# Performance work log

Hardware: AMD Instinct MI355X
Metric: run time of the kernel (lower is better)

## Reference

```python
import jax, jax.numpy as jnp
import numpy as np

N = 1_000_000
G = 32
CLAMP = 1e-4          # sigmoid_clamp
GAMMA = 2.0           # module-level gamma
FOCAL_ALPHA = 0.25    # cfg.MODEL.FCOS.LOSS_ALPHA
FOCAL_GAMMA = 2.0     # cfg.MODEL.FCOS.LOSS_GAMMA


def setup_inputs() -> dict:
    key = jax.random.key(0)
    k1, k2, k3, k4 = jax.random.split(key, 4)
    return {
        "logits_pred": jax.random.normal(k1, (N, 1), dtype=jnp.float32),
        "scores": jax.random.uniform(k2, (N, 1), dtype=jnp.float32),
        "IoUMap": jax.random.uniform(k3, (N, 1), dtype=jnp.float32),
        "is_in_boxes": jax.random.randint(k4, (N, G), 0, 2, dtype=jnp.int32),
        "num_pos_avg": 100,
    }


def reference(logits_pred, scores, IoUMap, is_in_boxes, num_pos_avg):
    f32 = jnp.float32
    mask = is_in_boxes > 0                                  # [N,G] bool
    any_mask = mask.any(axis=0)                             # [G]

    p = jnp.clip(jax.nn.sigmoid(logits_pred), CLAMP, 1.0 - CLAMP)  # box_pred [N,1]
    p0 = p[:, 0]                                            # [N]

    # alignment metrics: single class => scores[:, labels] broadcasts column 0
    am = scores[:, 0][:, None] * mask.astype(f32)           # [N,G]
    iou = jax.lax.stop_gradient(IoUMap)[:, 0][:, None] * mask.astype(f32)

    # per-box confidence = max of alignment metric over in-box locations
    conf = jnp.max(jnp.where(mask, am, -jnp.inf), axis=0)   # [G]
    conf = jnp.where(any_mask, conf, f32(0.0))

    am_safe = jnp.where(mask, am, f32(1.0))                 # avoid pow(0, c) grad issues
    raw = jnp.where(mask, jnp.power(am_safe, conf[None, :]) * iou, f32(0.0))

    # normalize(x) = (x + 1e-4) / (max(x) + 1e-4) over in-box subset
    mx = jnp.max(jnp.where(mask, raw, -jnp.inf), axis=0)    # [G]
    mx = jnp.where(any_mask, mx, f32(1.0))
    pos_w = jnp.where(mask & any_mask[None, :],
                      (raw + CLAMP) / (mx[None, :] + CLAMP), f32(0.0))  # [N,G]

    # negative mask: locations covered by no gt box (single-class case)
    neg_mask = ~mask.any(axis=1)                            # [N]
    neg_loss = jnp.sum(jnp.where(neg_mask,
                                 -jnp.log(1.0 - p0) * jnp.power(p0, FOCAL_GAMMA),
                                 f32(0.0))) * (1.0 - FOCAL_ALPHA)

    wmask = pos_w > 0.0
    wc = jnp.clip(pos_w, CLAMP, 1.0 - CLAMP)                # clamp applied at positive entries
    logp = jnp.log(p0)[:, None]
    log1mp = jnp.log(1.0 - p0)[:, None]
    pos_loss = -jnp.sum(jnp.where(wmask,
                                  logp * jnp.power(wc * (1.0 - p0)[:, None], GAMMA),
                                  f32(0.0))) * FOCAL_ALPHA
    box_neg_loss = -jnp.sum(jnp.where(wmask,
                                      log1mp * jnp.power((1.0 - wc) * p0[:, None], GAMMA),
                                      f32(0.0))) * FOCAL_ALPHA

    denom = jnp.asarray(num_pos_avg, f32)
    return (neg_loss + pos_loss + box_neg_loss) / denom
```

## Files before the change

kernel.cpp:

```cpp
#include <hip/hip_runtime.h>
#include <hip/hip_bf16.h>
#include <stdint.h>


constexpr float kClamp = 1e-4f;

__global__ void init_kernel(uint32_t* confbits, uint32_t* mxbits, float* out) {
    int t = threadIdx.x;
    if (t < 32) { confbits[t] = 0u; mxbits[t] = 0u; }
    if (t == 0) out[0] = 0.0f;
}

template <bool WRITE_BITS>
__global__ void pack_conf_kernel(const int4* __restrict__ boxes4,
                                 const float* __restrict__ scores,
                                 uint32_t* __restrict__ bits,
                                 uint32_t* __restrict__ confbits,
                                 long long nchunks) {
    __shared__ uint32_t conf_lds[32];
    int tid = threadIdx.x;
    if (tid < 32) conf_lds[tid] = 0u;
    __syncthreads();
    long long stride = (long long)gridDim.x * blockDim.x;
    for (long long c = (long long)blockIdx.x * blockDim.x + tid; c < nchunks; c += stride) {
        int4 v = boxes4[c];
        uint32_t nib = (uint32_t)(v.x > 0) | ((uint32_t)(v.y > 0) << 1) |
                       ((uint32_t)(v.z > 0) << 2) | ((uint32_t)(v.w > 0) << 3);
        int sub = (int)(c & 7);
        long long row = c >> 3;
        if (WRITE_BITS) {
            uint32_t r = nib << (sub * 4);
            r |= __shfl_xor(r, 1);
            r |= __shfl_xor(r, 2);
            r |= __shfl_xor(r, 4);
            if ((tid & 7) == 0) bits[row] = r;
        }
        if (nib) {
            uint32_t sb = __float_as_uint(scores[row]);
            int g0 = sub * 4;
            if (nib & 1u) atomicMax(&conf_lds[g0 + 0], sb);
            if (nib & 2u) atomicMax(&conf_lds[g0 + 1], sb);
            if (nib & 4u) atomicMax(&conf_lds[g0 + 2], sb);
            if (nib & 8u) atomicMax(&conf_lds[g0 + 3], sb);
        }
    }
    __syncthreads();
    if (tid < 32 && conf_lds[tid]) atomicMax(&confbits[tid], conf_lds[tid]);
}

__device__ inline uint32_t row_mask_from_boxes(const int4* __restrict__ boxes4, int row) {
    uint32_t m = 0;
#pragma unroll
    for (int k = 0; k < 8; ++k) {
        int4 v = boxes4[(long long)row * 8 + k];
        uint32_t nib = (uint32_t)(v.x > 0) | ((uint32_t)(v.y > 0) << 1) |
                       ((uint32_t)(v.z > 0) << 2) | ((uint32_t)(v.w > 0) << 3);
        m |= nib << (k * 4);
    }
    return m;
}

template <bool USE_BITS>
__global__ void mx_kernel(const uint32_t* __restrict__ bits,
                          const int4* __restrict__ boxes4,
                          const float* __restrict__ scores,
                          const float* __restrict__ iouMap,
                          const uint32_t* __restrict__ confbits,
                          uint32_t* __restrict__ mxbits, int n) {
    __shared__ float conf_lds[32];
    __shared__ uint32_t mx_lds[32];
    int tid = threadIdx.x;
    if (tid < 32) { conf_lds[tid] = __uint_as_float(confbits[tid]); mx_lds[tid] = 0u; }
    __syncthreads();
    int stride = gridDim.x * blockDim.x;
    for (int row = blockIdx.x * blockDim.x + tid; row < n; row += stride) {
        uint32_t m = USE_BITS ? bits[row] : row_mask_from_boxes(boxes4, row);
        if (!m) continue;
        float s = scores[row];
        float iou = iouMap[row];
        float l2s = log2f(s);
        while (m) {
            int g = __ffs(m) - 1;
            m &= m - 1;
            float t = conf_lds[g] * l2s;
            float e = exp2f(t);
            if (t != t) e = 1.0f;
            float raw = e * iou;
            atomicMax(&mx_lds[g], __float_as_uint(raw));
        }
    }
    __syncthreads();
    if (tid < 32 && mx_lds[tid]) atomicMax(&mxbits[tid], mx_lds[tid]);
}

template <bool USE_BITS>
__global__ void loss_kernel(const uint32_t* __restrict__ bits,
                            const int4* __restrict__ boxes4,
                            const float* __restrict__ logits,
                            const float* __restrict__ scores,
                            const float* __restrict__ iouMap,
                            const uint32_t* __restrict__ confbits,
                            const uint32_t* __restrict__ mxbits,
                            const void* __restrict__ denom_ptr,
                            float* __restrict__ out, int n) {
    __shared__ float conf_lds[32];
    __shared__ float mx_lds[32];
    __shared__ float wsum[4];
    int tid = threadIdx.x;
    if (tid < 32) {
        conf_lds[tid] = __uint_as_float(confbits[tid]);
        mx_lds[tid] = __uint_as_float(mxbits[tid]);
    }
    __syncthreads();
    float acc = 0.0f;
    int stride = gridDim.x * blockDim.x;
    for (int row = blockIdx.x * blockDim.x + tid; row < n; row += stride) {
        uint32_t m = USE_BITS ? bits[row] : row_mask_from_boxes(boxes4, row);
        float x = logits[row];
        float p = 1.0f / (1.0f + expf(-x));
        p = fminf(fmaxf(p, kClamp), 1.0f - kClamp);
        if (!m) {
            float l1mp = logf(1.0f - p);
            acc -= l1mp * p * p * 0.75f;
            continue;
        }
        float s = scores[row];
        float iou = iouMap[row];
        float l2s = log2f(s);
        float logp = logf(p);
        float log1mp = logf(1.0f - p);
        float omp = 1.0f - p;
        while (m) {
            int g = __ffs(m) - 1;
            m &= m - 1;
            float t = conf_lds[g] * l2s;
            float e = exp2f(t);
            if (t != t) e = 1.0f;
            float raw = e * iou;
            float wc = (raw + kClamp) / (mx_lds[g] + kClamp);
            wc = fminf(fmaxf(wc, kClamp), 1.0f - kClamp);
            float a1 = wc * omp;
            float a2 = (1.0f - wc) * p;
            acc -= (logp * a1 * a1 + log1mp * a2 * a2) * 0.25f;
        }
    }
    for (int off = 32; off > 0; off >>= 1) acc += __shfl_down(acc, off);
    if ((tid & 63) == 0) wsum[tid >> 6] = acc;
    __syncthreads();
    if (tid == 0) {
        int iv = *(const int*)denom_ptr;
        float fv = *(const float*)denom_ptr;
        float denom = (iv > 0 && iv < (1 << 24)) ? (float)iv : fv;
        float tot = (wsum[0] + wsum[1] + wsum[2] + wsum[3]) / denom;
        atomicAdd(out, tot);
    }
}

extern "C" void kernel_launch(void* const* d_in, const int* in_sizes, int n_in,
                              void* d_out, int out_size, void* d_ws, size_t ws_size,
                              hipStream_t stream) {
    const float* logits = (const float*)d_in[0];
    const float* scores = (const float*)d_in[1];
    const float* iou    = (const float*)d_in[2];
    const int4*  boxes4 = (const int4*)d_in[3];
    const void*  npa    = d_in[4];
    float* out = (float*)d_out;

    int n = in_sizes[0];
    long long gtotal = in_sizes[3];
    long long nchunks = gtotal / 4;

    uint32_t* confbits = (uint32_t*)d_ws;
    uint32_t* mxbits   = confbits + 32;
    uint32_t* bits     = confbits + 64;
    bool use_bits = ws_size >= (size_t)n * 4 + 256;

    init_kernel<<<1, 64, 0, stream>>>(confbits, mxbits, out);

    if (use_bits)
        pack_conf_kernel<true><<<2048, 256, 0, stream>>>(boxes4, scores, bits, confbits, nchunks);
    else
        pack_conf_kernel<false><<<2048, 256, 0, stream>>>(boxes4, scores, nullptr, confbits, nchunks);

    if (use_bits) {
        mx_kernel<true><<<2048, 256, 0, stream>>>(bits, nullptr, scores, iou, confbits, mxbits, n);
        loss_kernel<true><<<2048, 256, 0, stream>>>(bits, nullptr, logits, scores, iou,
                                                    confbits, mxbits, npa, out, n);
    } else {
        mx_kernel<false><<<2048, 256, 0, stream>>>(nullptr, boxes4, scores, iou, confbits, mxbits, n);
        loss_kernel<false><<<2048, 256, 0, stream>>>(nullptr, boxes4, logits, scores, iou,
                                                     confbits, mxbits, npa, out, n);
    }
}
```

Before: 286.9 us.

## Replace per-element LDS atomics with register max reductions in log domain

```diff
diff --git a/kernel.cpp b/kernel.cpp
--- a/kernel.cpp
+++ b/kernel.cpp
@@ -4,10 +4,20 @@
 
 
 constexpr float kClamp = 1e-4f;
-
-__global__ void init_kernel(uint32_t* confbits, uint32_t* mxbits, float* out) {
+constexpr uint32_t kNegInfKey = 0x007FFFFFu;
+
+__device__ inline uint32_t fkey(float f) {
+    uint32_t u = __float_as_uint(f);
+    return (u & 0x80000000u) ? ~u : (u | 0x80000000u);
+}
+__device__ inline float funkey(uint32_t k) {
+    uint32_t u = (k & 0x80000000u) ? (k ^ 0x80000000u) : ~k;
+    return __uint_as_float(u);
+}
+
+__global__ void init_kernel(uint32_t* confbits, uint32_t* mxkeys, float* out) {
     int t = threadIdx.x;
-    if (t < 32) { confbits[t] = 0u; mxbits[t] = 0u; }
+    if (t < 32) { confbits[t] = 0u; mxkeys[t] = kNegInfKey; }
     if (t == 0) out[0] = 0.0f;
 }
 
@@ -21,28 +31,38 @@
     int tid = threadIdx.x;
     if (tid < 32) conf_lds[tid] = 0u;
     __syncthreads();
+    int g0 = (tid & 7) * 4;
+    float r0 = 0.0f, r1 = 0.0f, r2 = 0.0f, r3 = 0.0f;
     long long stride = (long long)gridDim.x * blockDim.x;
     for (long long c = (long long)blockIdx.x * blockDim.x + tid; c < nchunks; c += stride) {
         int4 v = boxes4[c];
         uint32_t nib = (uint32_t)(v.x > 0) | ((uint32_t)(v.y > 0) << 1) |
                        ((uint32_t)(v.z > 0) << 2) | ((uint32_t)(v.w > 0) << 3);
-        int sub = (int)(c & 7);
         long long row = c >> 3;
         if (WRITE_BITS) {
-            uint32_t r = nib << (sub * 4);
+            uint32_t r = nib << ((tid & 7) * 4);
             r |= __shfl_xor(r, 1);
             r |= __shfl_xor(r, 2);
             r |= __shfl_xor(r, 4);
             if ((tid & 7) == 0) bits[row] = r;
         }
-        if (nib) {
-            uint32_t sb = __float_as_uint(scores[row]);
-            int g0 = sub * 4;
-            if (nib & 1u) atomicMax(&conf_lds[g0 + 0], sb);
-            if (nib & 2u) atomicMax(&conf_lds[g0 + 1], sb);
-            if (nib & 4u) atomicMax(&conf_lds[g0 + 2], sb);
-            if (nib & 8u) atomicMax(&conf_lds[g0 + 3], sb);
-        }
+        float s = scores[row];
+        r0 = (nib & 1u) ? fmaxf(r0, s) : r0;
+        r1 = (nib & 2u) ? fmaxf(r1, s) : r1;
+        r2 = (nib & 4u) ? fmaxf(r2, s) : r2;
+        r3 = (nib & 8u) ? fmaxf(r3, s) : r3;
+    }
+    for (int off = 8; off < 64; off <<= 1) {
+        r0 = fmaxf(r0, __shfl_xor(r0, off));
+        r1 = fmaxf(r1, __shfl_xor(r1, off));
+        r2 = fmaxf(r2, __shfl_xor(r2, off));
+        r3 = fmaxf(r3, __shfl_xor(r3, off));
+    }
+    if ((tid & 63) < 8) {
+        atomicMax(&conf_lds[g0 + 0], __float_as_uint(r0));
+        atomicMax(&conf_lds[g0 + 1], __float_as_uint(r1));
+        atomicMax(&conf_lds[g0 + 2], __float_as_uint(r2));
+        atomicMax(&conf_lds[g0 + 3], __float_as_uint(r3));
     }
     __syncthreads();
     if (tid < 32 && conf_lds[tid]) atomicMax(&confbits[tid], conf_lds[tid]);
@@ -66,31 +86,34 @@
                           const float* __restrict__ scores,
                           const float* __restrict__ iouMap,
                           const uint32_t* __restrict__ confbits,
-                          uint32_t* __restrict__ mxbits, int n) {
-    __shared__ float conf_lds[32];
-    __shared__ uint32_t mx_lds[32];
+                          uint32_t* __restrict__ mxkeys, int n) {
+    __shared__ float conf_s[32];
+    __shared__ uint32_t smax[32];
     int tid = threadIdx.x;
-    if (tid < 32) { conf_lds[tid] = __uint_as_float(confbits[tid]); mx_lds[tid] = 0u; }
-    __syncthreads();
+    if (tid < 32) { conf_s[tid] = __uint_as_float(confbits[tid]); smax[tid] = kNegInfKey; }
+    __syncthreads();
+    float lmax[32];
+#pragma unroll
+    for (int g = 0; g < 32; ++g) lmax[g] = -__builtin_inff();
     int stride = gridDim.x * blockDim.x;
     for (int row = blockIdx.x * blockDim.x + tid; row < n; row += stride) {
         uint32_t m = USE_BITS ? bits[row] : row_mask_from_boxes(boxes4, row);
         if (!m) continue;
-        float s = scores[row];
-        float iou = iouMap[row];
-        float l2s = log2f(s);
-        while (m) {
-            int g = __ffs(m) - 1;
-            m &= m - 1;
-            float t = conf_lds[g] * l2s;
-            float e = exp2f(t);
-            if (t != t) e = 1.0f;
-            float raw = e * iou;
-            atomicMax(&mx_lds[g], __float_as_uint(raw));
-        }
-    }
-    __syncthreads();
-    if (tid < 32 && mx_lds[tid]) atomicMax(&mxbits[tid], mx_lds[tid]);
+        float l2s = log2f(scores[row]);
+        float l2i = log2f(iouMap[row]);
+#pragma unroll
+        for (int g = 0; g < 32; ++g) {
+            float t0 = conf_s[g] * l2s;
+            t0 = (t0 != t0) ? 0.0f : t0;
+            float t = t0 + l2i;
+            lmax[g] = (m & (1u << g)) ? fmaxf(lmax[g], t) : lmax[g];
+        }
+    }
+#pragma unroll
+    for (int g = 0; g < 32; ++g)
+        atomicMax(&smax[g], fkey(lmax[g]));
+    __syncthreads();
+    if (tid < 32) atomicMax(&mxkeys[tid], smax[tid]);
 }
 
 template <bool USE_BITS>
@@ -100,16 +123,17 @@
                             const float* __restrict__ scores,
                             const float* __restrict__ iouMap,
                             const uint32_t* __restrict__ confbits,
-                            const uint32_t* __restrict__ mxbits,
+                            const uint32_t* __restrict__ mxkeys,
                             const void* __restrict__ denom_ptr,
                             float* __restrict__ out, int n) {
-    __shared__ float conf_lds[32];
-    __shared__ float mx_lds[32];
+    __shared__ float conf_s[32];
+    __shared__ float invmx[32];
     __shared__ float wsum[4];
     int tid = threadIdx.x;
     if (tid < 32) {
-        conf_lds[tid] = __uint_as_float(confbits[tid]);
-        mx_lds[tid] = __uint_as_float(mxbits[tid]);
+        conf_s[tid] = __uint_as_float(confbits[tid]);
+        float mx = exp2f(funkey(mxkeys[tid]));
+        invmx[tid] = 1.0f / (mx + kClamp);
     }
     __syncthreads();
     float acc = 0.0f;
@@ -120,24 +144,21 @@
         float p = 1.0f / (1.0f + expf(-x));
         p = fminf(fmaxf(p, kClamp), 1.0f - kClamp);
         if (!m) {
-            float l1mp = logf(1.0f - p);
-            acc -= l1mp * p * p * 0.75f;
+            acc -= logf(1.0f - p) * p * p * 0.75f;
             continue;
         }
-        float s = scores[row];
-        float iou = iouMap[row];
-        float l2s = log2f(s);
+        float l2s = log2f(scores[row]);
+        float l2i = log2f(iouMap[row]);
         float logp = logf(p);
         float log1mp = logf(1.0f - p);
         float omp = 1.0f - p;
         while (m) {
             int g = __ffs(m) - 1;
             m &= m - 1;
-            float t = conf_lds[g] * l2s;
-            float e = exp2f(t);
-            if (t != t) e = 1.0f;
-            float raw = e * iou;
-            float wc = (raw + kClamp) / (mx_lds[g] + kClamp);
+            float t0 = conf_s[g] * l2s;
+            t0 = (t0 != t0) ? 0.0f : t0;
+            float raw = exp2f(t0 + l2i);
+            float wc = (raw + kClamp) * invmx[g];
             wc = fminf(fmaxf(wc, kClamp), 1.0f - kClamp);
             float a1 = wc * omp;
             float a2 = (1.0f - wc) * p;
@@ -171,24 +192,21 @@
     long long nchunks = gtotal / 4;
 
     uint32_t* confbits = (uint32_t*)d_ws;
-    uint32_t* mxbits   = confbits + 32;
+    uint32_t* mxkeys   = confbits + 32;
     uint32_t* bits     = confbits + 64;
     bool use_bits = ws_size >= (size_t)n * 4 + 256;
 
-    init_kernel<<<1, 64, 0, stream>>>(confbits, mxbits, out);
-
-    if (use_bits)
+    init_kernel<<<1, 64, 0, stream>>>(confbits, mxkeys, out);
+
+    if (use_bits) {
         pack_conf_kernel<true><<<2048, 256, 0, stream>>>(boxes4, scores, bits, confbits, nchunks);
-    else
+        mx_kernel<true><<<2048, 256, 0, stream>>>(bits, nullptr, scores, iou, confbits, mxkeys, n);
+        loss_kernel<true><<<2048, 256, 0, stream>>>(bits, nullptr, logits, scores, iou,
+                                                    confbits, mxkeys, npa, out, n);
+    } else {
         pack_conf_kernel<false><<<2048, 256, 0, stream>>>(boxes4, scores, nullptr, confbits, nchunks);
-
-    if (use_bits) {
-        mx_kernel<true><<<2048, 256, 0, stream>>>(bits, nullptr, scores, iou, confbits, mxbits, n);
-        loss_kernel<true><<<2048, 256, 0, stream>>>(bits, nullptr, logits, scores, iou,
-                                                    confbits, mxbits, npa, out, n);
-    } else {
-        mx_kernel<false><<<2048, 256, 0, stream>>>(nullptr, boxes4, scores, iou, confbits, mxbits, n);
+        mx_kernel<false><<<2048, 256, 0, stream>>>(nullptr, boxes4, scores, iou, confbits, mxkeys, n);
         loss_kernel<false><<<2048, 256, 0, stream>>>(nullptr, boxes4, logits, scores, iou,
-                                                     confbits, mxbits, npa, out, n);
-    }
-}
+                                                     confbits, mxkeys, npa, out, n);
+    }
+}
```

After: 424.3 us. 47.9% more time.
